# Optimization experiments

Hardware: AMD Instinct MI355X
Metric: run time of the kernel (lower is better)

Reference implementation:

```python
import jax, jax.numpy as jnp
import numpy as np

B, S, DIN, DOUT = 4, 2048, 4096, 11008


def setup_inputs() -> dict:
    key = jax.random.key(0)
    k1, k2, k3, k4 = jax.random.split(key, 4)
    x = jax.random.normal(k1, (B, S, DIN), dtype=jnp.float32)
    # signed int8 quantized weights, stored as int32 for portability
    Wq = jax.random.randint(k2, (DOUT, DIN), -127, 128, dtype=jnp.int32)
    # per-output-channel scales (positive, clamped >= 1e-8 as in from_float)
    scale = jnp.maximum(jax.random.uniform(k3, (DOUT,), dtype=jnp.float32) * 0.02, 1e-8)
    b = jax.random.normal(k4, (DOUT,), dtype=jnp.float32)
    return {"x": x, "Wq": Wq, "scale": scale, "b": b}


def reference(x, Wq, scale, b):
    # dequantize: W[o, i] = Wq[o, i] * scale[o]
    W = Wq.astype(x.dtype) * scale[:, None].astype(x.dtype)
    # y = x @ W.T + bias  (leading dims flattened implicitly by einsum)
    y = jnp.einsum('bsi,oi->bso', x, W) + b.astype(x.dtype)
    # act_type == 'gelu' -> act_id = 1 (exact GELU, matching torch default)
    y = jax.nn.gelu(y, approximate=False)
    return y
```

## Files before the change

### kernel.cpp

```cpp
#include <hip/hip_runtime.h>
#include <cstdint>
#include <cstddef>


#define Msz 8192
#define Nsz 11008
#define Ksz 4096
#define BM 128
#define BN 128
#define BKB 64

typedef __attribute__((ext_vector_type(4))) int int4v;
typedef __attribute__((ext_vector_type(8))) short short8;
typedef __attribute__((ext_vector_type(4))) float floatx4;

__device__ __forceinline__ void async16(const void* g, void* l) {
  __builtin_amdgcn_global_load_lds(
      (const __attribute__((address_space(1))) void*)g,
      (__attribute__((address_space(3))) void*)l, 16, 0, 0);
}

__global__ __launch_bounds__(256) void quant_x(
    const float* __restrict__ x, signed char* __restrict__ xq,
    float* __restrict__ qs) {
  const int row = blockIdx.x;
  const int tid = threadIdx.x;
  const int lane = tid & 63;
  const int wave = tid >> 6;
  const float4* xr = (const float4*)(x + (size_t)row * Ksz);

  float4 v[4];
  float m = 0.f;
#pragma unroll
  for (int t = 0; t < 4; ++t) {
    v[t] = xr[tid + t * 256];
    m = fmaxf(m, fmaxf(fmaxf(fabsf(v[t].x), fabsf(v[t].y)),
                       fmaxf(fabsf(v[t].z), fabsf(v[t].w))));
  }
#pragma unroll
  for (int o = 32; o > 0; o >>= 1) m = fmaxf(m, __shfl_down(m, o));
  __shared__ float sm[4];
  if (lane == 0) sm[wave] = m;
  __syncthreads();
  const float am = fmaxf(fmaxf(sm[0], sm[1]), fmaxf(sm[2], sm[3]));
  const float rs = am > 0.f ? 127.0f / am : 0.f;
  if (tid == 0) qs[row] = am * (1.0f / 127.0f);

  unsigned* outd = (unsigned*)(xq + (size_t)row * Ksz);
#pragma unroll
  for (int t = 0; t < 4; ++t) {
    int q0 = __float2int_rn(fminf(fmaxf(v[t].x * rs, -127.f), 127.f));
    int q1 = __float2int_rn(fminf(fmaxf(v[t].y * rs, -127.f), 127.f));
    int q2 = __float2int_rn(fminf(fmaxf(v[t].z * rs, -127.f), 127.f));
    int q3 = __float2int_rn(fminf(fmaxf(v[t].w * rs, -127.f), 127.f));
    outd[tid + t * 256] = (unsigned)(q0 & 255) | ((unsigned)(q1 & 255) << 8) |
                          ((unsigned)(q2 & 255) << 16) | ((unsigned)q3 << 24);
  }
}

__global__ __launch_bounds__(256) void pack_w(const int4* __restrict__ w,
                                              unsigned* __restrict__ o) {
  const unsigned gid = blockIdx.x * 256 + threadIdx.x;
  const unsigned stride = 11008u * 256u;
#pragma unroll
  for (int t = 0; t < 4; ++t) {
    const unsigned idx = gid + t * stride;
    const int4 a = w[idx];
    o[idx] = (unsigned)(a.x & 255) | ((unsigned)(a.y & 255) << 8) |
             ((unsigned)(a.z & 255) << 16) | ((unsigned)a.w << 24);
  }
}

__global__ __launch_bounds__(256) void gemm_i8(
    const signed char* __restrict__ A8,
    const signed char* __restrict__ B8,
    const float* __restrict__ qs,
    const float* __restrict__ scale, const float* __restrict__ bias,
    float* __restrict__ out) {
  __shared__ signed char sA[BM * BKB];
  __shared__ signed char sB[BN * BKB];

  const int tid = threadIdx.x;
  const int wave = tid >> 6;
  const int lane = tid & 63;

  const int lbid = blockIdx.x;
  int bx, by;
  if (lbid < 5120) {
    const int p = lbid >> 9;
    const int r = lbid & 511;
    bx = p * 8 + (r >> 6);
    by = r & 63;
  } else {
    const int r = lbid - 5120;
    bx = 80 + (r >> 6);
    by = r & 63;
  }
  const int bn0 = bx * BN;
  const int bm0 = by * BM;
  const int mw = (wave >> 1) * 64;
  const int nw = (wave & 1) * 64;

  int4v acc[4][4];
#pragma unroll
  for (int i = 0; i < 4; ++i)
#pragma unroll
    for (int j = 0; j < 4; ++j) acc[i][j] = (int4v)0;

  const int chunk = (lane & 3) * 16;
  for (int k0 = 0; k0 < Ksz; k0 += BKB) {
#pragma unroll
    for (int iss = 0; iss < 2; ++iss) {
      const int row = wave * 32 + iss * 16 + (lane >> 2);
      async16(A8 + (size_t)(bm0 + row) * Ksz + k0 + chunk, &sA[row * BKB + chunk]);
      async16(B8 + (size_t)(bn0 + row) * Ksz + k0 + chunk, &sB[row * BKB + chunk]);
    }
    __syncthreads();

    int4v af[4], bfr[4];
    const int kof = (lane >> 4) * 16;
#pragma unroll
    for (int i = 0; i < 4; ++i) {
      af[i] = *(const int4v*)&sA[(mw + i * 16 + (lane & 15)) * BKB + kof];
      bfr[i] = *(const int4v*)&sB[(nw + i * 16 + (lane & 15)) * BKB + kof];
    }
#pragma unroll
    for (int i = 0; i < 4; ++i)
#pragma unroll
      for (int j = 0; j < 4; ++j)
        acc[i][j] =
            __builtin_amdgcn_mfma_i32_16x16x64_i8(af[i], bfr[j], acc[i][j], 0, 0, 0);
    __syncthreads();
  }

  float qsr[4][4];
#pragma unroll
  for (int i = 0; i < 4; ++i) {
    const int row0 = bm0 + mw + i * 16 + (lane >> 4) * 4;
#pragma unroll
    for (int r = 0; r < 4; ++r) qsr[i][r] = qs[row0 + r];
  }
#pragma unroll
  for (int j = 0; j < 4; ++j) {
    const int col = bn0 + nw + j * 16 + (lane & 15);
    const float s = scale[col];
    const float bb = bias[col];
#pragma unroll
    for (int i = 0; i < 4; ++i) {
      const int row0 = bm0 + mw + i * 16 + (lane >> 4) * 4;
#pragma unroll
      for (int r = 0; r < 4; ++r) {
        float v = (float)acc[i][j][r] * (qsr[i][r] * s) + bb;
        v = 0.5f * v * (1.0f + erff(v * 0.7071067811865476f));
        out[(size_t)(row0 + r) * Nsz + col] = v;
      }
    }
  }
}

__device__ __forceinline__ unsigned int f2bf(float f) {
  unsigned int u = __builtin_bit_cast(unsigned int, f);
  unsigned int r = u + 0x7FFFu + ((u >> 16) & 1u);
  return r >> 16;
}

__global__ __launch_bounds__(256) void gemm_bf16_inline(
    const float* __restrict__ Af, const int* __restrict__ Bi,
    const float* __restrict__ scale, const float* __restrict__ bias,
    float* __restrict__ out) {
  __shared__ unsigned short sA[BM * 32];
  __shared__ unsigned short sB[BN * 32];
  const int tid = threadIdx.x;
  const int wave = tid >> 6;
  const int lane = tid & 63;
  const int bn0 = blockIdx.x * BN;
  const int bm0 = blockIdx.y * BM;
  const int mw = (wave >> 1) * 64;
  const int nw = (wave & 1) * 64;
  floatx4 acc[4][4];
#pragma unroll
  for (int i = 0; i < 4; ++i)
#pragma unroll
    for (int j = 0; j < 4; ++j) acc[i][j] = (floatx4)0.f;
  for (int k0 = 0; k0 < Ksz; k0 += 32) {
#pragma unroll
    for (int it = 0; it < 4; ++it) {
      const int f = tid + it * 256;
      const int row = f >> 3;
      const int c4 = (f & 7) * 4;
      const float4 v = *(const float4*)(Af + (size_t)(bm0 + row) * Ksz + k0 + c4);
      uint2 p;
      p.x = f2bf(v.x) | (f2bf(v.y) << 16);
      p.y = f2bf(v.z) | (f2bf(v.w) << 16);
      *(uint2*)&sA[row * 32 + c4] = p;
      const int4 w = *(const int4*)(Bi + (size_t)(bm0 + row) * Ksz + k0 + c4);
      const int4 w2 = *(const int4*)(Bi + (size_t)(bn0 + row) * Ksz + k0 + c4);
      (void)w;
      uint2 q;
      q.x = f2bf((float)w2.x) | (f2bf((float)w2.y) << 16);
      q.y = f2bf((float)w2.z) | (f2bf((float)w2.w) << 16);
      *(uint2*)&sB[row * 32 + c4] = q;
    }
    __syncthreads();
    short8 af[4], bfr[4];
    const int kof2 = (lane >> 4) * 8;
#pragma unroll
    for (int i = 0; i < 4; ++i) {
      af[i] = *(const short8*)&sA[(mw + i * 16 + (lane & 15)) * 32 + kof2];
      bfr[i] = *(const short8*)&sB[(nw + i * 16 + (lane & 15)) * 32 + kof2];
    }
#pragma unroll
    for (int i = 0; i < 4; ++i)
#pragma unroll
      for (int j = 0; j < 4; ++j)
        acc[i][j] =
            __builtin_amdgcn_mfma_f32_16x16x32_bf16(af[i], bfr[j], acc[i][j], 0, 0, 0);
    __syncthreads();
  }
#pragma unroll
  for (int j = 0; j < 4; ++j) {
    const int col = bn0 + nw + j * 16 + (lane & 15);
    const float s = scale[col];
    const float bb = bias[col];
#pragma unroll
    for (int i = 0; i < 4; ++i) {
      const int row0 = bm0 + mw + i * 16 + (lane >> 4) * 4;
#pragma unroll
      for (int r = 0; r < 4; ++r) {
        float v = acc[i][j][r] * s + bb;
        v = 0.5f * v * (1.0f + erff(v * 0.7071067811865476f));
        out[(size_t)(row0 + r) * Nsz + col] = v;
      }
    }
  }
}

extern "C" void kernel_launch(void* const* d_in, const int* in_sizes, int n_in,
                              void* d_out, int out_size, void* d_ws, size_t ws_size,
                              hipStream_t stream) {
  const float* x = (const float*)d_in[0];
  const int* Wq = (const int*)d_in[1];
  const float* scale = (const float*)d_in[2];
  const float* bias = (const float*)d_in[3];
  float* out = (float*)d_out;

  const size_t nx = (size_t)Msz * Ksz;
  const size_t nwq = (size_t)Nsz * Ksz;
  const size_t need = nx + nwq + Msz * sizeof(float);

  if (ws_size >= need) {
    signed char* xq = (signed char*)d_ws;
    signed char* wp = xq + nx;
    float* qsd = (float*)(wp + nwq);
    quant_x<<<dim3(Msz), dim3(256), 0, stream>>>(x, xq, qsd);
    pack_w<<<dim3((unsigned)(nwq / (16 * 256))), dim3(256), 0, stream>>>(
        (const int4*)Wq, (unsigned*)wp);
    gemm_i8<<<dim3(Nsz / BN * (Msz / BM)), dim3(256), 0, stream>>>(
        xq, wp, qsd, scale, bias, out);
  } else {
    dim3 grid(Nsz / BN, Msz / BM);
    gemm_bf16_inline<<<grid, dim3(256), 0, stream>>>(x, Wq, scale, bias, out);
  }
}
```

Measured before the change: 1.163 ms.

## Rewrite int8 GEMM with 256x256 tiles, double-buffered swizzled LDS and phased prefetch

Replaces the 128x128, single-buffered int8 GEMM with a 512-thread, 256x256x128 tile kernel. It double-buffers A and B in LDS using an XOR-swizzled layout, and interleaves half-tile async global-to-LDS loads with MFMA phases using explicit waitcnt, barriers and setprio. It also remaps block IDs so neighbouring tiles are spread across the eight XCD groups. The goal is to hide global-load latency behind compute, raise data reuse per byte loaded and avoid LDS bank conflicts. In exchange it uses much more LDS and registers, which limits occupancy, and the hand-tuned waitcnt ordering is fragile.

```diff
diff --git a/kernel.cpp b/kernel.cpp
--- a/kernel.cpp
+++ b/kernel.cpp
@@ -6,9 +6,18 @@
 #define Msz 8192
 #define Nsz 11008
 #define Ksz 4096
+
+#define TM 256
+#define TN 256
+#define TK 128
+#define NT (Ksz / TK)
+#define NI (NT / 2)
+#define HALF (128 * TK)
+#define NWG ((Msz / TM) * (Nsz / TN))
+#define CPX (NWG / 8)
+
 #define BM 128
 #define BN 128
-#define BKB 64
 
 typedef __attribute__((ext_vector_type(4))) int int4v;
 typedef __attribute__((ext_vector_type(8))) short short8;
@@ -71,86 +80,126 @@
   }
 }
 
-__global__ __launch_bounds__(256) void gemm_i8(
+__device__ __forceinline__ void stage_half(signed char* dst,
+                                           const signed char* src, int grow0,
+                                           int kt, int tid) {
+  const int c = tid & 7;
+  const int k0 = kt * TK;
+#pragma unroll
+  for (int rho = 0; rho < 2; ++rho) {
+    const int rl = rho * 64 + (tid >> 3);
+    async16(src + (size_t)(grow0 + rl) * Ksz + k0 + ((c ^ (rl & 7)) << 4),
+            dst + rho * 8192 + tid * 16);
+  }
+}
+
+__device__ __forceinline__ int4v ldfrag(const signed char* s, int row,
+                                        int slot) {
+  return *(const int4v*)(s + row * TK + (((slot) ^ (row & 7)) << 4));
+}
+
+#define PHASE(b, q, LOADB, SDST, GSRC, GROW0, KT, VM)                        \
+  {                                                                          \
+    int4v afr[2][2];                                                         \
+    _Pragma("unroll") for (int ii = 0; ii < 2; ++ii) {                       \
+      const int ar = wr * 128 + ((2 * (q) + ii) << 4) + (lane & 15);         \
+      _Pragma("unroll") for (int kk = 0; kk < 2; ++kk)                       \
+          afr[ii][kk] = ldfrag(sA[b], ar, kk * 4 + (lane >> 4));             \
+    }                                                                        \
+    if (LOADB) {                                                             \
+      _Pragma("unroll") for (int jj = 0; jj < 4; ++jj) {                     \
+        const int br = wc * 64 + (jj << 4) + (lane & 15);                    \
+        _Pragma("unroll") for (int kk = 0; kk < 2; ++kk)                     \
+            bfr[jj][kk] = ldfrag(sB[b], br, kk * 4 + (lane >> 4));           \
+      }                                                                      \
+    }                                                                        \
+    stage_half(SDST, GSRC, GROW0, KT, tid);                                  \
+    if (LOADB) asm volatile("s_waitcnt lgkmcnt(8)" ::: "memory");            \
+    __builtin_amdgcn_s_barrier();                                            \
+    asm volatile("s_waitcnt lgkmcnt(0)" ::: "memory");                       \
+    __builtin_amdgcn_s_setprio(1);                                           \
+    _Pragma("unroll") for (int kk = 0; kk < 2; ++kk)                         \
+        _Pragma("unroll") for (int ii = 0; ii < 2; ++ii)                     \
+            _Pragma("unroll") for (int jj = 0; jj < 4; ++jj)                 \
+                acc[2 * (q) + ii][jj] =                                      \
+                    __builtin_amdgcn_mfma_i32_16x16x64_i8(                   \
+                        afr[ii][kk], bfr[jj][kk], acc[2 * (q) + ii][jj], 0,  \
+                        0, 0);                                               \
+    __builtin_amdgcn_s_setprio(0);                                           \
+    if (VM) asm volatile("s_waitcnt vmcnt(4)" ::: "memory");                 \
+    __builtin_amdgcn_s_barrier();                                            \
+  }
+
+__global__ __launch_bounds__(512, 2) void gemm_i8(
     const signed char* __restrict__ A8,
     const signed char* __restrict__ B8,
     const float* __restrict__ qs,
     const float* __restrict__ scale, const float* __restrict__ bias,
     float* __restrict__ out) {
-  __shared__ signed char sA[BM * BKB];
-  __shared__ signed char sB[BN * BKB];
+  __shared__ signed char sA[2][TM * TK];
+  __shared__ signed char sB[2][TN * TK];
 
   const int tid = threadIdx.x;
   const int wave = tid >> 6;
   const int lane = tid & 63;
-
-  const int lbid = blockIdx.x;
-  int bx, by;
-  if (lbid < 5120) {
-    const int p = lbid >> 9;
-    const int r = lbid & 511;
-    bx = p * 8 + (r >> 6);
-    by = r & 63;
-  } else {
-    const int r = lbid - 5120;
-    bx = 80 + (r >> 6);
-    by = r & 63;
-  }
-  const int bn0 = bx * BN;
-  const int bm0 = by * BM;
-  const int mw = (wave >> 1) * 64;
-  const int nw = (wave & 1) * 64;
-
-  int4v acc[4][4];
-#pragma unroll
-  for (int i = 0; i < 4; ++i)
+  const int wr = wave >> 2;
+  const int wc = wave & 3;
+
+  const int bid = blockIdx.x;
+  const int swz = (bid & 7) * CPX + (bid >> 3);
+  const int bm0 = (swz & 31) * TM;
+  const int bn0 = (swz >> 5) * TN;
+
+  int4v acc[8][4];
+#pragma unroll
+  for (int i = 0; i < 8; ++i)
 #pragma unroll
     for (int j = 0; j < 4; ++j) acc[i][j] = (int4v)0;
-
-  const int chunk = (lane & 3) * 16;
-  for (int k0 = 0; k0 < Ksz; k0 += BKB) {
-#pragma unroll
-    for (int iss = 0; iss < 2; ++iss) {
-      const int row = wave * 32 + iss * 16 + (lane >> 2);
-      async16(A8 + (size_t)(bm0 + row) * Ksz + k0 + chunk, &sA[row * BKB + chunk]);
-      async16(B8 + (size_t)(bn0 + row) * Ksz + k0 + chunk, &sB[row * BKB + chunk]);
-    }
-    __syncthreads();
-
-    int4v af[4], bfr[4];
-    const int kof = (lane >> 4) * 16;
-#pragma unroll
-    for (int i = 0; i < 4; ++i) {
-      af[i] = *(const int4v*)&sA[(mw + i * 16 + (lane & 15)) * BKB + kof];
-      bfr[i] = *(const int4v*)&sB[(nw + i * 16 + (lane & 15)) * BKB + kof];
-    }
-#pragma unroll
-    for (int i = 0; i < 4; ++i)
-#pragma unroll
-      for (int j = 0; j < 4; ++j)
-        acc[i][j] =
-            __builtin_amdgcn_mfma_i32_16x16x64_i8(af[i], bfr[j], acc[i][j], 0, 0, 0);
-    __syncthreads();
-  }
-
-  float qsr[4][4];
-#pragma unroll
-  for (int i = 0; i < 4; ++i) {
-    const int row0 = bm0 + mw + i * 16 + (lane >> 4) * 4;
-#pragma unroll
-    for (int r = 0; r < 4; ++r) qsr[i][r] = qs[row0 + r];
-  }
-#pragma unroll
-  for (int j = 0; j < 4; ++j) {
-    const int col = bn0 + nw + j * 16 + (lane & 15);
-    const float s = scale[col];
-    const float bb = bias[col];
-#pragma unroll
-    for (int i = 0; i < 4; ++i) {
-      const int row0 = bm0 + mw + i * 16 + (lane >> 4) * 4;
+  int4v bfr[4][2];
+
+  stage_half(sA[0], A8, bm0, 0, tid);
+  stage_half(sA[0] + HALF, A8, bm0 + 128, 0, tid);
+  stage_half(sB[0], B8, bn0, 0, tid);
+  stage_half(sB[0] + HALF, B8, bn0 + 128, 0, tid);
+  stage_half(sB[1], B8, bn0, 1, tid);
+  stage_half(sB[1] + HALF, B8, bn0 + 128, 1, tid);
+  asm volatile("s_waitcnt vmcnt(4)" ::: "memory");
+  __builtin_amdgcn_s_barrier();
+
+  for (int j = 0; j < NI; ++j) {
+    const int tA1 = 2 * j + 1;
+    const int tB2 = (2 * j + 2 < NT) ? 2 * j + 2 : NT - 1;
+    const int tB3 = (2 * j + 3 < NT) ? 2 * j + 3 : NT - 1;
+    PHASE(0, 0, true, sA[1], A8, bm0, tA1, false)
+    PHASE(0, 1, false, sA[1] + HALF, A8, bm0 + 128, tA1, false)
+    PHASE(0, 2, false, sB[0], B8, bn0, tB2, false)
+    PHASE(0, 3, false, sB[0] + HALF, B8, bn0 + 128, tB2, true)
+    PHASE(1, 0, true, sA[0], A8, bm0, tB2, false)
+    PHASE(1, 1, false, sA[0] + HALF, A8, bm0 + 128, tB2, false)
+    PHASE(1, 2, false, sB[1], B8, bn0, tB3, false)
+    PHASE(1, 3, false, sB[1] + HALF, B8, bn0 + 128, tB3, true)
+  }
+  asm volatile("s_waitcnt vmcnt(0)" ::: "memory");
+
+  float sc[4], bb[4];
+#pragma unroll
+  for (int jj = 0; jj < 4; ++jj) {
+    const int col = bn0 + wc * 64 + jj * 16 + (lane & 15);
+    sc[jj] = scale[col];
+    bb[jj] = bias[col];
+  }
+#pragma unroll
+  for (int i = 0; i < 8; ++i) {
+    const int row0 = bm0 + wr * 128 + i * 16 + (lane >> 4) * 4;
+    float qv[4];
+#pragma unroll
+    for (int r = 0; r < 4; ++r) qv[r] = qs[row0 + r];
+#pragma unroll
+    for (int jj = 0; jj < 4; ++jj) {
+      const int col = bn0 + wc * 64 + jj * 16 + (lane & 15);
 #pragma unroll
       for (int r = 0; r < 4; ++r) {
-        float v = (float)acc[i][j][r] * (qsr[i][r] * s) + bb;
+        float v = (float)acc[i][jj][r] * (qv[r] * sc[jj]) + bb[jj];
         v = 0.5f * v * (1.0f + erff(v * 0.7071067811865476f));
         out[(size_t)(row0 + r) * Nsz + col] = v;
       }
@@ -193,9 +242,7 @@
       p.x = f2bf(v.x) | (f2bf(v.y) << 16);
       p.y = f2bf(v.z) | (f2bf(v.w) << 16);
       *(uint2*)&sA[row * 32 + c4] = p;
-      const int4 w = *(const int4*)(Bi + (size_t)(bm0 + row) * Ksz + k0 + c4);
       const int4 w2 = *(const int4*)(Bi + (size_t)(bn0 + row) * Ksz + k0 + c4);
-      (void)w;
       uint2 q;
       q.x = f2bf((float)w2.x) | (f2bf((float)w2.y) << 16);
       q.y = f2bf((float)w2.z) | (f2bf((float)w2.w) << 16);
@@ -255,8 +302,7 @@
     quant_x<<<dim3(Msz), dim3(256), 0, stream>>>(x, xq, qsd);
     pack_w<<<dim3((unsigned)(nwq / (16 * 256))), dim3(256), 0, stream>>>(
         (const int4*)Wq, (unsigned*)wp);
-    gemm_i8<<<dim3(Nsz / BN * (Msz / BM)), dim3(256), 0, stream>>>(
-        xq, wp, qsd, scale, bias, out);
+    gemm_i8<<<dim3(NWG), dim3(512), 0, stream>>>(xq, wp, qsd, scale, bias, out);
   } else {
     dim3 grid(Nsz / BN, Msz / BM);
     gemm_bf16_inline<<<grid, dim3(256), 0, stream>>>(x, Wq, scale, bias, out);
```

After: 1.137 ms. 1.02x faster.
